# Optimization experiments

Measured on AMD Instinct MI355X. Metric: run time of the kernel, lower is better.

The kernel has to match this reference:

```python
import math
import jax, jax.numpy as jnp
import numpy as np

CHUNK_LEN = 64
NUM_HEADS = 16
HIDDEN = 1024
HEAD = HIDDEN // NUM_HEADS


def setup_inputs() -> dict:
    key = jax.random.key(0)
    ks = jax.random.split(key, 8)
    B, S, C, N, L = 4, 2048, 32, 2, 128
    scale = 1.0 / math.sqrt(HIDDEN)
    return {
        "query": jax.random.normal(ks[0], (B, S, HIDDEN), jnp.float32),
        "kv": jax.random.normal(ks[1], (B, C, N, L, HIDDEN), jnp.float32),
        "Wq": jax.random.normal(ks[2], (HIDDEN, HIDDEN), jnp.float32) * scale,
        "bq": jnp.zeros((HIDDEN,), jnp.float32),
        "Wk": jax.random.normal(ks[3], (HIDDEN, HIDDEN), jnp.float32) * scale,
        "bk": jnp.zeros((HIDDEN,), jnp.float32),
        "Wv": jax.random.normal(ks[4], (HIDDEN, HIDDEN), jnp.float32) * scale,
        "bv": jnp.zeros((HIDDEN,), jnp.float32),
    }


def reference(query, kv, Wq, bq, Wk, bk, Wv, bv):
    B, S, H = query.shape
    _, C, N, L, _ = kv.shape
    # shift query right by chunk_len-1 and pad to n_chunks*chunk_len
    q = query[:, CHUNK_LEN - 1:]
    add_len = C * CHUNK_LEN - q.shape[1]
    q = jnp.pad(q, ((0, 0), (0, add_len), (0, 0)))
    q = q.reshape(B, C, CHUNK_LEN, H)
    q = (q @ Wq.T + bq).reshape(B, C, CHUNK_LEN, NUM_HEADS, HEAD)
    k = (kv @ Wk.T + bk).reshape(B, C, N, L, NUM_HEADS, HEAD)
    v = (kv @ Wv.T + bv).reshape(B, C, N, L, NUM_HEADS, HEAD)
    # scores: [B, C, heads, chunk_len, N, L]
    attn = jnp.einsum("bcihd,bcnjhd->bchinj", q, k) / math.sqrt(HEAD)
    # softmax over flattened neighbor dims (n, j)
    attn = jax.nn.softmax(attn.reshape(B, C, NUM_HEADS, CHUNK_LEN, N * L), axis=-1)
    attn = attn.reshape(B, C, NUM_HEADS, CHUNK_LEN, N, L)
    h = jnp.einsum("bchinj,bcnjhd->bcihd", attn, v).reshape(B, C * CHUNK_LEN, H)
    # shift left: prepend chunk_len-1 zeros, truncate to seq_len
    h = jnp.pad(h, ((0, 0), (CHUNK_LEN - 1, 0), (0, 0)))[:, :S]
    return h
```

## Files before the change

kernel.cpp:

```cpp
#include <hip/hip_runtime.h>
#include <hip/hip_bf16.h>
#include <stdint.h>

#define HD 1024
#define SEQ 2048
#define NC 32

typedef __bf16 bf16x4 __attribute__((ext_vector_type(4)));
typedef __bf16 bf16x8 __attribute__((ext_vector_type(8)));
typedef float f32x4 __attribute__((ext_vector_type(4)));

__device__ inline unsigned short f2bf(float f) {
  union { float f; unsigned int u; } v; v.f = f;
  unsigned int r = v.u + 0x7fffu + ((v.u >> 16) & 1u);
  return (unsigned short)(r >> 16);
}
__device__ inline unsigned int pkcvt(float a, float b) {
  __hip_bfloat162 h = __float22bfloat162_rn(make_float2(a, b));
  union { __hip_bfloat162 h; unsigned int u; } v; v.h = h;
  return v.u;
}
__device__ inline uint4 pack8(float4 x, float4 y) {
  return make_uint4(pkcvt(x.x, x.y), pkcvt(x.z, x.w), pkcvt(y.x, y.y), pkcvt(y.z, y.w));
}
__device__ inline bf16x8 ld_frag8(const unsigned short* p) {
  bf16x4 lo = *(const bf16x4*)p;
  bf16x4 hi = *(const bf16x4*)(p + 4);
  return __builtin_shufflevector(lo, hi, 0, 1, 2, 3, 4, 5, 6, 7);
}
__device__ inline void glds16(const unsigned short* g, unsigned short* l) {
  __builtin_amdgcn_global_load_lds(
      (const __attribute__((address_space(1))) unsigned int*)g,
      (__attribute__((address_space(3))) unsigned int*)l, 16, 0, 0);
}

__global__ __launch_bounds__(256) void zero_head_kernel(float* __restrict__ out) {
  int i = (blockIdx.x * 256 + threadIdx.x) * 4;
  int b = i / 64512;
  int r = i - b * 64512;
  *(float4*)(out + (size_t)b * (SEQ * HD) + r) = make_float4(0.f, 0.f, 0.f, 0.f);
}

__global__ __launch_bounds__(256) void cvt_kernel(const float* __restrict__ in,
                                                  unsigned short* __restrict__ out, int n8) {
  int i = blockIdx.x * 256 + threadIdx.x;
  if (i < n8) {
    float4 a = ((const float4*)in)[(size_t)i * 2];
    float4 b = ((const float4*)in)[(size_t)i * 2 + 1];
    ((uint4*)out)[i] = pack8(a, b);
  }
}

__global__ __launch_bounds__(256, 2) void gemm_kv_kernel(
    const float* __restrict__ A, const unsigned short* __restrict__ Wkb,
    const unsigned short* __restrict__ Wvb, const float* __restrict__ bk,
    const float* __restrict__ bv, unsigned short* __restrict__ Kp,
    unsigned short* __restrict__ Vt) {
  __shared__ unsigned short lds_a[128 * 32];
  __shared__ unsigned short lds_bk[128 * 32];
  __shared__ unsigned short lds_bv[128 * 32];
  const int t = threadIdx.x;
  const int l = t & 63, w = t >> 6;
  const int wm = w >> 1, wn = w & 1;
  const int lr = l & 15, lq = l >> 4;
  const int bid = blockIdx.x;
  const int xcd = bid & 7, local = bid >> 3;
  const int nblk = local & 7, mblk = xcd * 32 + (local >> 3);
  const size_t arow0 = (size_t)mblk * 128;
  const size_t brow0 = (size_t)nblk * 128;
  const int c0 = t, c1 = 256 + t;
  const float* a0 = A + (arow0 + (c0 >> 2)) * HD + (c0 & 3) * 8;
  const float* a1 = A + (arow0 + (c1 >> 2)) * HD + (c1 & 3) * 8;
  const unsigned short* bk0 = Wkb + (brow0 + (c0 >> 2)) * HD + (c0 & 3) * 8;
  const unsigned short* bk1 = Wkb + (brow0 + (c1 >> 2)) * HD + (c1 & 3) * 8;
  const unsigned short* bv0 = Wvb + (brow0 + (c0 >> 2)) * HD + (c0 & 3) * 8;
  const unsigned short* bv1 = Wvb + (brow0 + (c1 >> 2)) * HD + (c1 & 3) * 8;

  f32x4 acck[4][4], accv[4][4];
  for (int i = 0; i < 4; i++)
    for (int j = 0; j < 4; j++) {
      acck[i][j] = (f32x4){0.f, 0.f, 0.f, 0.f};
      accv[i][j] = (f32x4){0.f, 0.f, 0.f, 0.f};
    }

  for (int kk = 0; kk < 32; ++kk) {
    const int k0 = kk * 32;
    __syncthreads();
    glds16(bk0 + k0, lds_bk + c0 * 8);
    glds16(bk1 + k0, lds_bk + c1 * 8);
    glds16(bv0 + k0, lds_bv + c0 * 8);
    glds16(bv1 + k0, lds_bv + c1 * 8);
    {
      float4 x0 = *(const float4*)(a0 + k0), y0 = *(const float4*)(a0 + k0 + 4);
      float4 x1 = *(const float4*)(a1 + k0), y1 = *(const float4*)(a1 + k0 + 4);
      *(uint4*)(lds_a + c0 * 8) = pack8(x0, y0);
      *(uint4*)(lds_a + c1 * 8) = pack8(x1, y1);
    }
    __syncthreads();
    bf16x8 af[4], bkf[4], bvf[4];
    for (int mt = 0; mt < 4; ++mt)
      af[mt] = *(const bf16x8*)(lds_a + (wm * 64 + mt * 16 + lr) * 32 + lq * 8);
    for (int nt = 0; nt < 4; ++nt) {
      bkf[nt] = *(const bf16x8*)(lds_bk + (wn * 64 + nt * 16 + lr) * 32 + lq * 8);
      bvf[nt] = *(const bf16x8*)(lds_bv + (wn * 64 + nt * 16 + lr) * 32 + lq * 8);
    }
    for (int mt = 0; mt < 4; ++mt)
      for (int nt = 0; nt < 4; ++nt) {
        acck[mt][nt] = __builtin_amdgcn_mfma_f32_16x16x32_bf16(af[mt], bkf[nt], acck[mt][nt], 0, 0, 0);
        accv[mt][nt] = __builtin_amdgcn_mfma_f32_16x16x32_bf16(af[mt], bvf[nt], accv[mt][nt], 0, 0, 0);
      }
  }

  for (int nt = 0; nt < 4; ++nt) {
    int n = nblk * 128 + wn * 64 + nt * 16 + lr;
    float bkk = bk[n], bvv = bv[n];
    int h = n >> 6, d = n & 63;
    for (int mt = 0; mt < 4; ++mt) {
      size_t mbase = arow0 + wm * 64 + mt * 16 + lq * 4;
      for (int r = 0; r < 4; ++r)
        Kp[(mbase + r) * HD + n] = f2bf(acck[mt][nt][r] + bkk);
      size_t bc = mbase >> 8, j = mbase & 255;
      *(ushort4*)(Vt + ((bc * 16 + h) * 64 + d) * 256 + j) =
          make_ushort4(f2bf(accv[mt][nt][0] + bvv), f2bf(accv[mt][nt][1] + bvv),
                       f2bf(accv[mt][nt][2] + bvv), f2bf(accv[mt][nt][3] + bvv));
    }
  }
}

__global__ __launch_bounds__(256, 2) void gemm_q_kernel(
    const float* __restrict__ A, const unsigned short* __restrict__ Wqb,
    const float* __restrict__ bq, unsigned short* __restrict__ Qp) {
  __shared__ unsigned short lds_a[128 * 32];
  __shared__ unsigned short lds_b[128 * 32];
  const int t = threadIdx.x;
  const int l = t & 63, w = t >> 6;
  const int wm = w >> 1, wn = w & 1;
  const int lr = l & 15, lq = l >> 4;
  const int bid = blockIdx.x;
  const int xcd = bid & 7, local = bid >> 3;
  const int nblk = local & 7, mblk = xcd * 8 + (local >> 3);
  const size_t arow0 = (size_t)mblk * 128;
  const size_t brow0 = (size_t)nblk * 128;
  const int c0 = t, c1 = 256 + t;
  const unsigned short* b0 = Wqb + (brow0 + (c0 >> 2)) * HD + (c0 & 3) * 8;
  const unsigned short* b1 = Wqb + (brow0 + (c1 >> 2)) * HD + (c1 & 3) * 8;
  size_t g0 = arow0 + (c0 >> 2), g1 = arow0 + (c1 >> 2);
  int t0 = (int)(g0 & 2047), t1 = (int)(g1 & 2047);
  bool v0 = t0 < 1985, v1 = t1 < 1985;
  const float* a0 = A + ((g0 & ~(size_t)2047) + t0 + 63) * HD + (c0 & 3) * 8;
  const float* a1 = A + ((g1 & ~(size_t)2047) + t1 + 63) * HD + (c1 & 3) * 8;

  f32x4 acc[4][4];
  for (int i = 0; i < 4; i++)
    for (int j = 0; j < 4; j++) acc[i][j] = (f32x4){0.f, 0.f, 0.f, 0.f};

  for (int kk = 0; kk < 32; ++kk) {
    const int k0 = kk * 32;
    __syncthreads();
    glds16(b0 + k0, lds_b + c0 * 8);
    glds16(b1 + k0, lds_b + c1 * 8);
    {
      uint4 p0 = make_uint4(0, 0, 0, 0), p1 = make_uint4(0, 0, 0, 0);
      if (v0) p0 = pack8(*(const float4*)(a0 + k0), *(const float4*)(a0 + k0 + 4));
      if (v1) p1 = pack8(*(const float4*)(a1 + k0), *(const float4*)(a1 + k0 + 4));
      *(uint4*)(lds_a + c0 * 8) = p0;
      *(uint4*)(lds_a + c1 * 8) = p1;
    }
    __syncthreads();
    bf16x8 af[4], bfr[4];
    for (int mt = 0; mt < 4; ++mt)
      af[mt] = *(const bf16x8*)(lds_a + (wm * 64 + mt * 16 + lr) * 32 + lq * 8);
    for (int nt = 0; nt < 4; ++nt)
      bfr[nt] = *(const bf16x8*)(lds_b + (wn * 64 + nt * 16 + lr) * 32 + lq * 8);
    for (int mt = 0; mt < 4; ++mt)
      for (int nt = 0; nt < 4; ++nt)
        acc[mt][nt] = __builtin_amdgcn_mfma_f32_16x16x32_bf16(af[mt], bfr[nt], acc[mt][nt], 0, 0, 0);
  }

  for (int nt = 0; nt < 4; ++nt) {
    int n = nblk * 128 + wn * 64 + nt * 16 + lr;
    float bvv = bq[n];
    for (int mt = 0; mt < 4; ++mt) {
      size_t mbase = arow0 + wm * 64 + mt * 16 + lq * 4;
      for (int r = 0; r < 4; ++r)
        Qp[(mbase + r) * HD + n] = f2bf(acc[mt][nt][r] + bvv);
    }
  }
}

#define QK_STRIDE 68
#define P_STRIDE 260

__global__ __launch_bounds__(256, 3) void attn_kernel(
    const unsigned short* __restrict__ Qp, const unsigned short* __restrict__ Kp,
    const unsigned short* __restrict__ Vt, float* __restrict__ out) {
  __shared__ unsigned short q_s[64 * QK_STRIDE];
  __shared__ unsigned short k_s[256 * QK_STRIDE];
  const int t = threadIdx.x;
  const int l = t & 63, w = t >> 6;
  const int lr = l & 15, lq = l >> 4;
  const int bid = blockIdx.x;
  const int head = bid & 15, cc = (bid >> 4) & 31, b = bid >> 9;
  const size_t qrow0 = (size_t)(b * NC + cc) * 64;
  const size_t kvrow0 = (size_t)(b * NC + cc) * 256;
  const int hcol = head * 64;
  const unsigned short* vbase = Vt + ((size_t)((b * NC + cc) * 16 + head) * 64) * 256;

  for (int p = 0; p < 4; ++p) {
    int chunk = p * 256 + t;
    int row = chunk >> 4, c4 = (chunk & 15) * 4;
    *(uint2*)(q_s + row * QK_STRIDE + c4) = *(const uint2*)(Qp + (qrow0 + row) * HD + hcol + c4);
  }
  for (int p = 0; p < 16; ++p) {
    int chunk = p * 256 + t;
    int row = chunk >> 4, c4 = (chunk & 15) * 4;
    *(uint2*)(k_s + row * QK_STRIDE + c4) = *(const uint2*)(Kp + (kvrow0 + row) * HD + hcol + c4);
  }
  __syncthreads();

  bf16x8 qa0 = ld_frag8(q_s + (w * 16 + lr) * QK_STRIDE + lq * 8);
  bf16x8 qa1 = ld_frag8(q_s + (w * 16 + lr) * QK_STRIDE + 32 + lq * 8);
  f32x4 sc[16];
  for (int nt = 0; nt < 16; ++nt) {
    bf16x8 kb0 = ld_frag8(k_s + (nt * 16 + lr) * QK_STRIDE + lq * 8);
    bf16x8 kb1 = ld_frag8(k_s + (nt * 16 + lr) * QK_STRIDE + 32 + lq * 8);
    f32x4 a = (f32x4){0.f, 0.f, 0.f, 0.f};
    a = __builtin_amdgcn_mfma_f32_16x16x32_bf16(qa0, kb0, a, 0, 0, 0);
    a = __builtin_amdgcn_mfma_f32_16x16x32_bf16(qa1, kb1, a, 0, 0, 0);
    sc[nt] = a;
  }
  float mrow[4] = {-1e30f, -1e30f, -1e30f, -1e30f};
  for (int nt = 0; nt < 16; ++nt)
    for (int r = 0; r < 4; ++r) mrow[r] = fmaxf(mrow[r], sc[nt][r]);
  for (int off = 1; off < 16; off <<= 1)
    for (int r = 0; r < 4; ++r) mrow[r] = fmaxf(mrow[r], __shfl_xor(mrow[r], off, 16));
  float srow[4] = {0.f, 0.f, 0.f, 0.f};
  const float cexp = 0.18033688011112042f;
  for (int nt = 0; nt < 16; ++nt)
    for (int r = 0; r < 4; ++r) {
      float p = exp2f((sc[nt][r] - mrow[r]) * cexp);
      sc[nt][r] = p;
      srow[r] += p;
    }
  for (int off = 1; off < 16; off <<= 1)
    for (int r = 0; r < 4; ++r) srow[r] += __shfl_xor(srow[r], off, 16);

  __syncthreads();

  for (int nt = 0; nt < 16; ++nt)
    for (int r = 0; r < 4; ++r)
      k_s[(w * 16 + lq * 4 + r) * P_STRIDE + nt * 16 + lr] = f2bf(sc[nt][r]);

  f32x4 o[4];
  for (int i = 0; i < 4; ++i) o[i] = (f32x4){0.f, 0.f, 0.f, 0.f};
  for (int ks = 0; ks < 8; ++ks) {
    bf16x8 pa = ld_frag8(k_s + (w * 16 + lr) * P_STRIDE + ks * 32 + lq * 8);
    for (int nt2 = 0; nt2 < 4; ++nt2) {
      bf16x8 vb = *(const bf16x8*)(vbase + (size_t)(nt2 * 16 + lr) * 256 + ks * 32 + lq * 8);
      o[nt2] = __builtin_amdgcn_mfma_f32_16x16x32_bf16(pa, vb, o[nt2], 0, 0, 0);
    }
  }

  for (int r = 0; r < 4; ++r) {
    int strip = w * 16 + lq * 4 + r;
    int trow = cc * 64 + strip;
    if (trow < 1985) {
      size_t orow = (size_t)b * SEQ + trow + 63;
      float inv = 1.0f / srow[r];
      for (int nt2 = 0; nt2 < 4; ++nt2)
        out[orow * HD + hcol + nt2 * 16 + lr] = o[nt2][r] * inv;
    }
  }
}

extern "C" void kernel_launch(void* const* d_in, const int* in_sizes, int n_in,
                              void* d_out, int out_size, void* d_ws, size_t ws_size,
                              hipStream_t stream) {
  (void)in_sizes; (void)n_in; (void)out_size; (void)ws_size;
  const float* query = (const float*)d_in[0];
  const float* kv    = (const float*)d_in[1];
  const float* Wq    = (const float*)d_in[2];
  const float* bq    = (const float*)d_in[3];
  const float* Wk    = (const float*)d_in[4];
  const float* bk    = (const float*)d_in[5];
  const float* Wv    = (const float*)d_in[6];
  const float* bv    = (const float*)d_in[7];
  float* out = (float*)d_out;

  unsigned short* Qp  = (unsigned short*)d_ws;
  unsigned short* Kp  = Qp + (size_t)8192 * 1024;
  unsigned short* Vt  = Kp + (size_t)32768 * 1024;
  unsigned short* Wqb = Vt + (size_t)32768 * 1024;
  unsigned short* Wkb = Wqb + (size_t)1024 * 1024;
  unsigned short* Wvb = Wkb + (size_t)1024 * 1024;

  zero_head_kernel<<<dim3(252), dim3(256), 0, stream>>>(out);
  cvt_kernel<<<dim3(512), dim3(256), 0, stream>>>(Wq, Wqb, 131072);
  cvt_kernel<<<dim3(512), dim3(256), 0, stream>>>(Wk, Wkb, 131072);
  cvt_kernel<<<dim3(512), dim3(256), 0, stream>>>(Wv, Wvb, 131072);
  gemm_q_kernel<<<dim3(512), dim3(256), 0, stream>>>(query, Wqb, bq, Qp);
  gemm_kv_kernel<<<dim3(2048), dim3(256), 0, stream>>>(kv, Wkb, Wvb, bk, bv, Kp, Vt);
  attn_kernel<<<dim3(2048), dim3(256), 0, stream>>>(Qp, Kp, Vt, out);
}
```

Measured before the change: 535.9 us.

## Halve KV GEMM N-tile, fuse weight conversions, load Q/K fragments directly

Result: no change. 545.0 us (+1.7%).

```diff
diff --git a/kernel.cpp b/kernel.cpp
--- a/kernel.cpp
+++ b/kernel.cpp
@@ -41,14 +41,16 @@
   *(float4*)(out + (size_t)b * (SEQ * HD) + r) = make_float4(0.f, 0.f, 0.f, 0.f);
 }
 
-__global__ __launch_bounds__(256) void cvt_kernel(const float* __restrict__ in,
-                                                  unsigned short* __restrict__ out, int n8) {
+__global__ __launch_bounds__(256) void cvt3_kernel(const float* __restrict__ Wq,
+                                                   const float* __restrict__ Wk,
+                                                   const float* __restrict__ Wv,
+                                                   unsigned short* __restrict__ out) {
   int i = blockIdx.x * 256 + threadIdx.x;
-  if (i < n8) {
-    float4 a = ((const float4*)in)[(size_t)i * 2];
-    float4 b = ((const float4*)in)[(size_t)i * 2 + 1];
-    ((uint4*)out)[i] = pack8(a, b);
-  }
+  int wsel = i >> 17, j = i & 131071;
+  const float* src = (wsel == 0) ? Wq : (wsel == 1) ? Wk : Wv;
+  float4 a = ((const float4*)src)[(size_t)j * 2];
+  float4 b = ((const float4*)src)[(size_t)j * 2 + 1];
+  ((uint4*)out)[i] = pack8(a, b);
 }
 
 __global__ __launch_bounds__(256, 2) void gemm_kv_kernel(
@@ -57,28 +59,26 @@
     const float* __restrict__ bv, unsigned short* __restrict__ Kp,
     unsigned short* __restrict__ Vt) {
   __shared__ unsigned short lds_a[128 * 32];
-  __shared__ unsigned short lds_bk[128 * 32];
-  __shared__ unsigned short lds_bv[128 * 32];
+  __shared__ unsigned short lds_bk[64 * 32];
+  __shared__ unsigned short lds_bv[64 * 32];
   const int t = threadIdx.x;
   const int l = t & 63, w = t >> 6;
   const int wm = w >> 1, wn = w & 1;
   const int lr = l & 15, lq = l >> 4;
   const int bid = blockIdx.x;
   const int xcd = bid & 7, local = bid >> 3;
-  const int nblk = local & 7, mblk = xcd * 32 + (local >> 3);
+  const int nblk = local & 15, mblk = xcd * 32 + (local >> 4);
   const size_t arow0 = (size_t)mblk * 128;
-  const size_t brow0 = (size_t)nblk * 128;
+  const size_t brow0 = (size_t)nblk * 64;
   const int c0 = t, c1 = 256 + t;
   const float* a0 = A + (arow0 + (c0 >> 2)) * HD + (c0 & 3) * 8;
   const float* a1 = A + (arow0 + (c1 >> 2)) * HD + (c1 & 3) * 8;
-  const unsigned short* bk0 = Wkb + (brow0 + (c0 >> 2)) * HD + (c0 & 3) * 8;
-  const unsigned short* bk1 = Wkb + (brow0 + (c1 >> 2)) * HD + (c1 & 3) * 8;
-  const unsigned short* bv0 = Wvb + (brow0 + (c0 >> 2)) * HD + (c0 & 3) * 8;
-  const unsigned short* bv1 = Wvb + (brow0 + (c1 >> 2)) * HD + (c1 & 3) * 8;
-
-  f32x4 acck[4][4], accv[4][4];
+  const unsigned short* bkp = Wkb + (brow0 + (t >> 2)) * HD + (t & 3) * 8;
+  const unsigned short* bvp = Wvb + (brow0 + (t >> 2)) * HD + (t & 3) * 8;
+
+  f32x4 acck[4][2], accv[4][2];
   for (int i = 0; i < 4; i++)
-    for (int j = 0; j < 4; j++) {
+    for (int j = 0; j < 2; j++) {
       acck[i][j] = (f32x4){0.f, 0.f, 0.f, 0.f};
       accv[i][j] = (f32x4){0.f, 0.f, 0.f, 0.f};
     }
@@ -86,10 +86,8 @@
   for (int kk = 0; kk < 32; ++kk) {
     const int k0 = kk * 32;
     __syncthreads();
-    glds16(bk0 + k0, lds_bk + c0 * 8);
-    glds16(bk1 + k0, lds_bk + c1 * 8);
-    glds16(bv0 + k0, lds_bv + c0 * 8);
-    glds16(bv1 + k0, lds_bv + c1 * 8);
+    glds16(bkp + k0, lds_bk + t * 8);
+    glds16(bvp + k0, lds_bv + t * 8);
     {
       float4 x0 = *(const float4*)(a0 + k0), y0 = *(const float4*)(a0 + k0 + 4);
       float4 x1 = *(const float4*)(a1 + k0), y1 = *(const float4*)(a1 + k0 + 4);
@@ -97,22 +95,22 @@
       *(uint4*)(lds_a + c1 * 8) = pack8(x1, y1);
     }
     __syncthreads();
-    bf16x8 af[4], bkf[4], bvf[4];
+    bf16x8 af[4], bkf[2], bvf[2];
     for (int mt = 0; mt < 4; ++mt)
       af[mt] = *(const bf16x8*)(lds_a + (wm * 64 + mt * 16 + lr) * 32 + lq * 8);
-    for (int nt = 0; nt < 4; ++nt) {
-      bkf[nt] = *(const bf16x8*)(lds_bk + (wn * 64 + nt * 16 + lr) * 32 + lq * 8);
-      bvf[nt] = *(const bf16x8*)(lds_bv + (wn * 64 + nt * 16 + lr) * 32 + lq * 8);
-    }
-    for (int mt = 0; mt < 4; ++mt)
-      for (int nt = 0; nt < 4; ++nt) {
+    for (int nt = 0; nt < 2; ++nt) {
+      bkf[nt] = *(const bf16x8*)(lds_bk + (wn * 32 + nt * 16 + lr) * 32 + lq * 8);
+      bvf[nt] = *(const bf16x8*)(lds_bv + (wn * 32 + nt * 16 + lr) * 32 + lq * 8);
+    }
+    for (int mt = 0; mt < 4; ++mt)
+      for (int nt = 0; nt < 2; ++nt) {
         acck[mt][nt] = __builtin_amdgcn_mfma_f32_16x16x32_bf16(af[mt], bkf[nt], acck[mt][nt], 0, 0, 0);
         accv[mt][nt] = __builtin_amdgcn_mfma_f32_16x16x32_bf16(af[mt], bvf[nt], accv[mt][nt], 0, 0, 0);
       }
   }
 
-  for (int nt = 0; nt < 4; ++nt) {
-    int n = nblk * 128 + wn * 64 + nt * 16 + lr;
+  for (int nt = 0; nt < 2; ++nt) {
+    int n = nblk * 64 + wn * 32 + nt * 16 + lr;
     float bkk = bk[n], bvv = bv[n];
     int h = n >> 6, d = n & 63;
     for (int mt = 0; mt < 4; ++mt) {
@@ -188,14 +186,12 @@
   }
 }
 
-#define QK_STRIDE 68
 #define P_STRIDE 260
 
 __global__ __launch_bounds__(256, 3) void attn_kernel(
     const unsigned short* __restrict__ Qp, const unsigned short* __restrict__ Kp,
     const unsigned short* __restrict__ Vt, float* __restrict__ out) {
-  __shared__ unsigned short q_s[64 * QK_STRIDE];
-  __shared__ unsigned short k_s[256 * QK_STRIDE];
+  __shared__ unsigned short p_s[64 * P_STRIDE];
   const int t = threadIdx.x;
   const int l = t & 63, w = t >> 6;
   const int lr = l & 15, lq = l >> 4;
@@ -206,24 +202,16 @@
   const int hcol = head * 64;
   const unsigned short* vbase = Vt + ((size_t)((b * NC + cc) * 16 + head) * 64) * 256;
 
-  for (int p = 0; p < 4; ++p) {
-    int chunk = p * 256 + t;
-    int row = chunk >> 4, c4 = (chunk & 15) * 4;
-    *(uint2*)(q_s + row * QK_STRIDE + c4) = *(const uint2*)(Qp + (qrow0 + row) * HD + hcol + c4);
-  }
-  for (int p = 0; p < 16; ++p) {
-    int chunk = p * 256 + t;
-    int row = chunk >> 4, c4 = (chunk & 15) * 4;
-    *(uint2*)(k_s + row * QK_STRIDE + c4) = *(const uint2*)(Kp + (kvrow0 + row) * HD + hcol + c4);
-  }
-  __syncthreads();
-
-  bf16x8 qa0 = ld_frag8(q_s + (w * 16 + lr) * QK_STRIDE + lq * 8);
-  bf16x8 qa1 = ld_frag8(q_s + (w * 16 + lr) * QK_STRIDE + 32 + lq * 8);
+  const unsigned short* qrow = Qp + (qrow0 + w * 16 + lr) * HD + hcol;
+  bf16x8 qa0 = *(const bf16x8*)(qrow + lq * 8);
+  bf16x8 qa1 = *(const bf16x8*)(qrow + 32 + lq * 8);
+
+  const unsigned short* kbase = Kp + kvrow0 * HD + hcol;
   f32x4 sc[16];
   for (int nt = 0; nt < 16; ++nt) {
-    bf16x8 kb0 = ld_frag8(k_s + (nt * 16 + lr) * QK_STRIDE + lq * 8);
-    bf16x8 kb1 = ld_frag8(k_s + (nt * 16 + lr) * QK_STRIDE + 32 + lq * 8);
+    const unsigned short* kr = kbase + (size_t)(nt * 16 + lr) * HD;
+    bf16x8 kb0 = *(const bf16x8*)(kr + lq * 8);
+    bf16x8 kb1 = *(const bf16x8*)(kr + 32 + lq * 8);
     f32x4 a = (f32x4){0.f, 0.f, 0.f, 0.f};
     a = __builtin_amdgcn_mfma_f32_16x16x32_bf16(qa0, kb0, a, 0, 0, 0);
     a = __builtin_amdgcn_mfma_f32_16x16x32_bf16(qa1, kb1, a, 0, 0, 0);
@@ -245,16 +233,14 @@
   for (int off = 1; off < 16; off <<= 1)
     for (int r = 0; r < 4; ++r) srow[r] += __shfl_xor(srow[r], off, 16);
 
-  __syncthreads();
-
   for (int nt = 0; nt < 16; ++nt)
     for (int r = 0; r < 4; ++r)
-      k_s[(w * 16 + lq * 4 + r) * P_STRIDE + nt * 16 + lr] = f2bf(sc[nt][r]);
+      p_s[(w * 16 + lq * 4 + r) * P_STRIDE + nt * 16 + lr] = f2bf(sc[nt][r]);
 
   f32x4 o[4];
   for (int i = 0; i < 4; ++i) o[i] = (f32x4){0.f, 0.f, 0.f, 0.f};
   for (int ks = 0; ks < 8; ++ks) {
-    bf16x8 pa = ld_frag8(k_s + (w * 16 + lr) * P_STRIDE + ks * 32 + lq * 8);
+    bf16x8 pa = ld_frag8(p_s + (w * 16 + lr) * P_STRIDE + ks * 32 + lq * 8);
     for (int nt2 = 0; nt2 < 4; ++nt2) {
       bf16x8 vb = *(const bf16x8*)(vbase + (size_t)(nt2 * 16 + lr) * 256 + ks * 32 + lq * 8);
       o[nt2] = __builtin_amdgcn_mfma_f32_16x16x32_bf16(pa, vb, o[nt2], 0, 0, 0);
@@ -295,10 +281,8 @@
   unsigned short* Wvb = Wkb + (size_t)1024 * 1024;
 
   zero_head_kernel<<<dim3(252), dim3(256), 0, stream>>>(out);
-  cvt_kernel<<<dim3(512), dim3(256), 0, stream>>>(Wq, Wqb, 131072);
-  cvt_kernel<<<dim3(512), dim3(256), 0, stream>>>(Wk, Wkb, 131072);
-  cvt_kernel<<<dim3(512), dim3(256), 0, stream>>>(Wv, Wvb, 131072);
+  cvt3_kernel<<<dim3(1536), dim3(256), 0, stream>>>(Wq, Wk, Wv, Wqb);
   gemm_q_kernel<<<dim3(512), dim3(256), 0, stream>>>(query, Wqb, bq, Qp);
-  gemm_kv_kernel<<<dim3(2048), dim3(256), 0, stream>>>(kv, Wkb, Wvb, bk, bv, Kp, Vt);
+  gemm_kv_kernel<<<dim3(4096), dim3(256), 0, stream>>>(kv, Wkb, Wvb, bk, bv, Kp, Vt);
   attn_kernel<<<dim3(2048), dim3(256), 0, stream>>>(Qp, Kp, Vt, out);
 }
```
